# Kernel tuning notes

Hardware: AMD Instinct MI355X
Metric: run time of the kernel (lower is better)

The kernel has to match this reference:

```python
import jax, jax.numpy as jnp
import numpy as np

B, L, D = 1, 1024, 1024
NL = 4            # n_layers
N = 16            # d_state
DI = 2 * D        # d_inner (expand=2)
DTR = (D + 15) // 16  # dt_rank = ceil(d_model/16) = 64
K = 4             # depthwise conv kernel size
EPS = 1e-5


def setup_inputs() -> dict:
    key = jax.random.key(0)
    ks = jax.random.split(key, 8)
    s = lambda k, shp, sc: jax.random.normal(k, shp, jnp.float32) * sc
    x = s(ks[0], (B, L, D), 1.0)
    norm_w = jnp.ones((NL, D), jnp.float32)
    in_w = s(ks[1], (NL, 2 * DI, D), D ** -0.5)          # in_proj (no bias)
    conv_w = s(ks[2], (NL, DI, K), 0.5)                   # depthwise conv1d weight
    conv_b = s(ks[3], (NL, DI), 0.02)                     # conv1d bias
    xproj_w = s(ks[4], (NL, DTR + 2 * N, DI), DI ** -0.5) # x_proj (no bias)
    dt_w = s(ks[5], (NL, DI, DTR), DTR ** -0.5)           # dt_proj weight
    dt_b = jnp.full((NL, DI), 0.1, jnp.float32)           # dt_proj bias (positive-ish delta)
    A_log = jnp.log(jnp.tile(jnp.arange(1, N + 1, dtype=jnp.float32), (NL, DI, 1)))  # [NL, DI, N]
    D_skip = jnp.ones((NL, DI), jnp.float32)
    out_w = s(ks[6], (NL, D, DI), DI ** -0.5)             # out_proj (no bias)
    return dict(x=x, norm_w=norm_w, in_w=in_w, conv_w=conv_w, conv_b=conv_b,
                xproj_w=xproj_w, dt_w=dt_w, dt_b=dt_b, A_log=A_log,
                D_skip=D_skip, out_w=out_w)


def _rmsnorm(x, w):
    return x * jax.lax.rsqrt(jnp.mean(x * x, axis=-1, keepdims=True) + EPS) * w


def _causal_depthwise_conv(u, w, b):
    # u: [B, L, DI], w: [DI, K], b: [DI]; causal (left pad K-1)
    up = jnp.pad(u, ((0, 0), (K - 1, 0), (0, 0)))
    y = b
    for k in range(K):
        y = y + up[:, k:k + L, :] * w[:, k]
    return y


def _selective_scan(dA, dBu, C):
    # dA, dBu: [B, L, DI, N]; C: [B, L, N]
    def step(h, inp):
        a, bu, c = inp
        h = a * h + bu                       # [B, DI, N]
        y = jnp.einsum('bdn,bn->bd', h, c)   # [B, DI]
        return h, y
    h0 = jnp.zeros((dA.shape[0], DI, N), dA.dtype)
    _, ys = jax.lax.scan(step, h0, (dA.transpose(1, 0, 2, 3),
                                    dBu.transpose(1, 0, 2, 3),
                                    C.transpose(1, 0, 2)))
    return ys.transpose(1, 0, 2)             # [B, L, DI]


def _mamba_block(x, p):
    norm_w, in_w, conv_w, conv_b, xproj_w, dt_w, dt_b, A_log, D_skip, out_w = p
    xn = _rmsnorm(x, norm_w)
    xz = jnp.einsum('bld,ed->ble', xn, in_w)             # [B, L, 2*DI]
    u, z = jnp.split(xz, 2, axis=-1)
    u = jax.nn.silu(_causal_depthwise_conv(u, conv_w, conv_b))
    x_dbl = jnp.einsum('bld,ed->ble', u, xproj_w)        # [B, L, DTR+2N]
    dt_r, Bt, Ct = jnp.split(x_dbl, [DTR, DTR + N], axis=-1)
    delta = jax.nn.softplus(jnp.einsum('blr,dr->bld', dt_r, dt_w) + dt_b)  # [B, L, DI]
    A = -jnp.exp(A_log)                                  # [DI, N]
    dA = jnp.exp(delta[..., None] * A)                   # [B, L, DI, N]
    dBu = delta[..., None] * Bt[:, :, None, :] * u[..., None]
    y = _selective_scan(dA, dBu, Ct) + u * D_skip        # [B, L, DI]
    y = y * jax.nn.silu(z)
    return x + jnp.einsum('ble,de->bld', y, out_w)       # residual


def reference(x, norm_w, in_w, conv_w, conv_b, xproj_w, dt_w, dt_b, A_log, D_skip, out_w):
    params = (norm_w, in_w, conv_w, conv_b, xproj_w, dt_w, dt_b, A_log, D_skip, out_w)
    out, _ = jax.lax.scan(lambda h, p: (_mamba_block(h, p), None), x, params)
    return out
```

## Files before the change

kernel.cpp:

```cpp
#include <hip/hip_runtime.h>
#include <hip/hip_bf16.h>
#include <stdint.h>

#define L 1024
#define D 1024
#define NLAYER 4
#define NSTATE 16
#define DI 2048
#define DTR 64
#define KCONV 4
#define XD 96
#define NC 64
#define CT 16
#define KSPLIT 16
#define OSPLIT 4
#define BK 32
#define DIST 4

typedef __attribute__((ext_vector_type(8))) short short8;
typedef __attribute__((ext_vector_type(4))) float floatx4;

__device__ __forceinline__ float siluf(float x) { return x / (1.f + __expf(-x)); }

__device__ __forceinline__ unsigned short f2bf(float x) {
    __hip_bfloat16 b = __float2bfloat16(x);
    return *reinterpret_cast<unsigned short*>(&b);
}

__device__ __forceinline__ short8 pack8(floatx4 a, floatx4 b) {
    short8 o;
    o[0] = (short)f2bf(a.x); o[1] = (short)f2bf(a.y);
    o[2] = (short)f2bf(a.z); o[3] = (short)f2bf(a.w);
    o[4] = (short)f2bf(b.x); o[5] = (short)f2bf(b.y);
    o[6] = (short)f2bf(b.z); o[7] = (short)f2bf(b.w);
    return o;
}

__device__ __forceinline__ void st_dev_u32(uint32_t* p, uint32_t v) {
    __hip_atomic_store(p, v, __ATOMIC_RELAXED, __HIP_MEMORY_SCOPE_AGENT);
}
__device__ __forceinline__ uint32_t ld_dev_u32(const uint32_t* p) {
    return __hip_atomic_load(p, __ATOMIC_RELAXED, __HIP_MEMORY_SCOPE_AGENT);
}
__device__ __forceinline__ void st_dev_u64(void* p, uint64_t v) {
    __hip_atomic_store((unsigned long long*)p, (unsigned long long)v, __ATOMIC_RELAXED, __HIP_MEMORY_SCOPE_AGENT);
}
__device__ __forceinline__ uint64_t ld_dev_u64(const void* p) {
    return (uint64_t)__hip_atomic_load((const unsigned long long*)p, __ATOMIC_RELAXED, __HIP_MEMORY_SCOPE_AGENT);
}
__device__ __forceinline__ float ld_dev_f(const float* p) {
    uint32_t u = ld_dev_u32((const uint32_t*)p);
    union { uint32_t u; float f; } c; c.u = u;
    return c.f;
}
__device__ __forceinline__ void st_dev_f(float* p, float v) {
    union { float f; uint32_t u; } c; c.f = v;
    st_dev_u32((uint32_t*)p, c.u);
}

#define BARRIER_NODRAIN() asm volatile("s_waitcnt lgkmcnt(0)\n\ts_barrier" ::: "memory")

__global__ __launch_bounds__(256) void rmsnorm_kernel(const float* __restrict__ x,
                                                      const float* __restrict__ w,
                                                      __hip_bfloat16* __restrict__ xn,
                                                      uint32_t* __restrict__ flags) {
    if (blockIdx.x == 0) {
#pragma unroll
        for (int i = 0; i < 3; ++i) st_dev_u32(&flags[threadIdx.x + i * 256], 0u);
    }
    int row = blockIdx.x;
    const float* xr = x + (size_t)row * D;
    float v[4];
    float s = 0.f;
#pragma unroll
    for (int i = 0; i < 4; ++i) {
        v[i] = xr[threadIdx.x + i * 256];
        s += v[i] * v[i];
    }
#pragma unroll
    for (int off = 32; off > 0; off >>= 1) s += __shfl_xor(s, off, 64);
    __shared__ float red[4];
    int wave = threadIdx.x >> 6;
    if ((threadIdx.x & 63) == 0) red[wave] = s;
    __syncthreads();
    float inv = rsqrtf((red[0] + red[1] + red[2] + red[3]) * (1.f / D) + 1e-5f);
#pragma unroll
    for (int i = 0; i < 4; ++i) {
        int c = threadIdx.x + i * 256;
        xn[(size_t)row * D + c] = __float2bfloat16(v[i] * inv * w[c]);
    }
}

template <int EPI, int ITERS, bool AF32, int QD>
__global__ __launch_bounds__(256, 2) void gemm_pipe(
    const void* __restrict__ Aptr, int lda,
    const float* __restrict__ Bw, int ldb, int Brows,
    float* __restrict__ C, int ldc, int Nvalid,
    const float* __restrict__ bias) {
    __shared__ __align__(16) __hip_bfloat16 As[2][128 * BK];
    __shared__ __align__(16) __hip_bfloat16 Bs[2][64 * BK];
    int tid = threadIdx.x;
    int wave = tid >> 6, lane = tid & 63;

    int gxy = gridDim.x * gridDim.y;
    int total = gxy * gridDim.z;
    int flat = (blockIdx.z * gridDim.y + blockIdx.y) * gridDim.x + blockIdx.x;
    int bm, bn, bz;
    if ((total & 7) == 0) {
        int lid = (flat & 7) * (total >> 3) + (flat >> 3);
        bz = lid / gxy;
        int rem = lid - bz * gxy;
        bn = rem / gridDim.y;
        bm = rem - bn * gridDim.y;
    } else {
        bm = blockIdx.y; bn = blockIdx.x; bz = blockIdx.z;
    }

    int m0 = bm * 128, n0 = bn * 64;
    int k_base = bz * (ITERS * BK);
    int wr = wave >> 1, wc = wave & 1;
    int srow = lane >> 2, scol = (lane & 3) * 8;
    int q = lane >> 4, r = lane & 15;

    floatx4 acc[4][2] = {};

    int arow0 = m0 + wave * 32 + srow;
    const __hip_bfloat16* gA0 = nullptr; const __hip_bfloat16* gA1 = nullptr;
    const float* gAf0 = nullptr; const float* gAf1 = nullptr;
    if (AF32) {
        gAf0 = (const float*)Aptr + (long)arow0 * lda + scol + k_base;
        gAf1 = gAf0 + (long)16 * lda;
    } else {
        gA0 = (const __hip_bfloat16*)Aptr + (long)arow0 * lda + scol + k_base;
        gA1 = gA0 + (long)16 * lda;
    }
    int bnrow = n0 + wave * 16 + srow;
    const float* gB = Bw + (long)bnrow * ldb + scol + k_base;
    bool bok = bnrow < Brows;

    short8 qa0[QD], qa1[QD];
    floatx4 qaf[AF32 ? QD : 1][4];
    floatx4 qb0[QD] = {}, qb1[QD] = {};

    auto ld = [&](int j) {
        int k0 = j * BK;
        int s = j & (QD - 1);
        if (AF32) {
            qaf[s][0] = *(const floatx4*)(gAf0 + k0);
            qaf[s][1] = *(const floatx4*)(gAf0 + k0 + 4);
            qaf[s][2] = *(const floatx4*)(gAf1 + k0);
            qaf[s][3] = *(const floatx4*)(gAf1 + k0 + 4);
        } else {
            qa0[s] = *(const short8*)(gA0 + k0);
            qa1[s] = *(const short8*)(gA1 + k0);
        }
        if (bok) {
            qb0[s] = *(const floatx4*)(gB + k0);
            qb1[s] = *(const floatx4*)(gB + k0 + 4);
        }
    };
    auto wrstage = [&](int j) {
        int p = j & 1, s = j & (QD - 1);
        if (AF32) {
            *(short8*)(&As[p][(wave * 32 + srow) * BK + scol]) = pack8(qaf[s][0], qaf[s][1]);
            *(short8*)(&As[p][(wave * 32 + 16 + srow) * BK + scol]) = pack8(qaf[s][2], qaf[s][3]);
        } else {
            *(short8*)(&As[p][(wave * 32 + srow) * BK + scol]) = qa0[s];
            *(short8*)(&As[p][(wave * 32 + 16 + srow) * BK + scol]) = qa1[s];
        }
        *(short8*)(&Bs[p][(wave * 16 + srow) * BK + scol]) = pack8(qb0[s], qb1[s]);
    };

#pragma unroll
    for (int j = 0; j < QD; ++j)
        if (j < ITERS) ld(j);
    wrstage(0);

#pragma unroll
    for (int k = 0; k < ITERS; ++k) {
        BARRIER_NODRAIN();
        if (k + QD < ITERS) ld(k + QD);
        if (k + 1 < ITERS) wrstage(k + 1);
        const short* Ap = (const short*)As[k & 1];
        const short* Bp = (const short*)Bs[k & 1];
        short8 af[4], bfr[2];
#pragma unroll
        for (int i = 0; i < 4; ++i)
            af[i] = *(const short8*)(Ap + (wr * 64 + i * 16 + r) * BK + q * 8);
#pragma unroll
        for (int j = 0; j < 2; ++j)
            bfr[j] = *(const short8*)(Bp + (wc * 32 + j * 16 + r) * BK + q * 8);
#pragma unroll
        for (int i = 0; i < 4; ++i)
#pragma unroll
            for (int j = 0; j < 2; ++j)
                acc[i][j] = __builtin_amdgcn_mfma_f32_16x16x32_bf16(af[i], bfr[j], acc[i][j], 0, 0, 0);
    }

#pragma unroll
    for (int i = 0; i < 4; ++i) {
        int mrow = m0 + wr * 64 + i * 16 + q * 4;
#pragma unroll
        for (int j = 0; j < 2; ++j) {
            int ncol = n0 + wc * 32 + j * 16 + r;
            if (ncol < Nvalid) {
#pragma unroll
                for (int rr = 0; rr < 4; ++rr) {
                    float v = acc[i][j][rr];
                    int m = mrow + rr;
                    if (EPI == 1) {
                        v += bias[ncol];
                        v = v > 20.f ? v : log1pf(__expf(v));
                    }
                    if (EPI == 2) atomicAdd(&C[(long)m * ldc + ncol], v);
                    else C[(long)m * ldc + ncol] = v;
                }
            }
        }
    }
}

template <int ITERS>
__global__ __launch_bounds__(256, 1) void gemm128(
    const __hip_bfloat16* __restrict__ A, int lda,
    const float* __restrict__ Bw, int ldb, int Brows,
    float* __restrict__ C, int ldc, long zstride) {
    __shared__ __align__(16) __hip_bfloat16 As[2][128 * BK];
    __shared__ __align__(16) __hip_bfloat16 Bs[2][128 * BK];
    int tid = threadIdx.x;
    int wave = tid >> 6, lane = tid & 63;

    int gxy = gridDim.x * gridDim.y;
    int total = gxy * gridDim.z;
    int flat = (blockIdx.z * gridDim.y + blockIdx.y) * gridDim.x + blockIdx.x;
    int bm, bn, bz;
    if ((total & 7) == 0) {
        int lid = (flat & 7) * (total >> 3) + (flat >> 3);
        bz = lid / gxy;
        int rem = lid - bz * gxy;
        bn = rem / gridDim.y;
        bm = rem - bn * gridDim.y;
    } else {
        bm = blockIdx.y; bn = blockIdx.x; bz = blockIdx.z;
    }

    int m0 = bm * 128, n0 = bn * 128;
    int k_base = bz * (ITERS * BK);
    C += (long)bz * zstride;
    int wr = wave >> 1, wc = wave & 1;
    int srow = lane >> 2, scol = (lane & 3) * 8;
    int q = lane >> 4, r = lane & 15;

    floatx4 acc[4][4] = {};

    const __hip_bfloat16* gA0 = A + (long)(m0 + wave * 32 + srow) * lda + scol + k_base;
    const __hip_bfloat16* gA1 = gA0 + (long)16 * lda;
    int bn0 = n0 + wave * 32 + srow;
    const float* gB0 = Bw + (long)bn0 * ldb + scol + k_base;
    const float* gB1 = gB0 + (long)16 * ldb;
    bool bok0 = bn0 < Brows, bok1 = (bn0 + 16) < Brows;

    short8 qa0[DIST], qa1[DIST];
    floatx4 qb0[DIST] = {}, qb1[DIST] = {}, qb2[DIST] = {}, qb3[DIST] = {};

    auto ld = [&](int j) {
        int k0 = j * BK;
        int s = j & (DIST - 1);
        qa0[s] = *(const short8*)(gA0 + k0);
        qa1[s] = *(const short8*)(gA1 + k0);
        if (bok0) {
            qb0[s] = *(const floatx4*)(gB0 + k0);
            qb1[s] = *(const floatx4*)(gB0 + k0 + 4);
        }
        if (bok1) {
            qb2[s] = *(const floatx4*)(gB1 + k0);
            qb3[s] = *(const floatx4*)(gB1 + k0 + 4);
        }
    };
    auto wrstage = [&](int j) {
        int p = j & 1, s = j & (DIST - 1);
        *(short8*)(&As[p][(wave * 32 + srow) * BK + scol]) = qa0[s];
        *(short8*)(&As[p][(wave * 32 + 16 + srow) * BK + scol]) = qa1[s];
        *(short8*)(&Bs[p][(wave * 32 + srow) * BK + scol]) = pack8(qb0[s], qb1[s]);
        *(short8*)(&Bs[p][(wave * 32 + 16 + srow) * BK + scol]) = pack8(qb2[s], qb3[s]);
    };

#pragma unroll
    for (int j = 0; j < DIST; ++j)
        if (j < ITERS) ld(j);
    wrstage(0);

#pragma unroll
    for (int k = 0; k < ITERS; ++k) {
        BARRIER_NODRAIN();
        if (k + DIST < ITERS) ld(k + DIST);
        if (k + 1 < ITERS) wrstage(k + 1);
        const short* Ap = (const short*)As[k & 1];
        const short* Bp = (const short*)Bs[k & 1];
        short8 af[4], bfr[4];
#pragma unroll
        for (int i = 0; i < 4; ++i)
            af[i] = *(const short8*)(Ap + (wr * 64 + i * 16 + r) * BK + q * 8);
#pragma unroll
        for (int j = 0; j < 4; ++j)
            bfr[j] = *(const short8*)(Bp + (wc * 64 + j * 16 + r) * BK + q * 8);
#pragma unroll
        for (int i = 0; i < 4; ++i)
#pragma unroll
            for (int j = 0; j < 4; ++j)
                acc[i][j] = __builtin_amdgcn_mfma_f32_16x16x32_bf16(af[i], bfr[j], acc[i][j], 0, 0, 0);
    }

#pragma unroll
    for (int i = 0; i < 4; ++i) {
        int mrow = m0 + wr * 64 + i * 16 + q * 4;
#pragma unroll
        for (int j = 0; j < 4; ++j) {
            int ncol = n0 + wc * 64 + j * 16 + r;
#pragma unroll
            for (int rr = 0; rr < 4; ++rr)
                C[(long)(mrow + rr) * ldc + ncol] = acc[i][j][rr];
        }
    }
}

template <int NPART, bool NORM>
__global__ __launch_bounds__(256) void reduce_kernel(const float* __restrict__ part2,
                                                     const float* __restrict__ xin,
                                                     const float* __restrict__ nw,
                                                     float* __restrict__ out,
                                                     __hip_bfloat16* __restrict__ xn) {
    int row = blockIdx.x;
    const float* xr = xin + (size_t)row * D;
    float v[4];
    float ss = 0.f;
#pragma unroll
    for (int i = 0; i < 4; ++i) {
        int c = threadIdx.x + i * 256;
        float s = xr[c];
#pragma unroll
        for (int p = 0; p < NPART; ++p)
            s += part2[(size_t)p * L * D + (size_t)row * D + c];
        v[i] = s;
        out[(size_t)row * D + c] = s;
        ss += s * s;
    }
    if (NORM) {
#pragma unroll
        for (int off = 32; off > 0; off >>= 1) ss += __shfl_xor(ss, off, 64);
        __shared__ float red[4];
        int wave = threadIdx.x >> 6;
        if ((threadIdx.x & 63) == 0) red[wave] = ss;
        __syncthreads();
        float inv = rsqrtf((red[0] + red[1] + red[2] + red[3]) * (1.f / D) + 1e-5f);
#pragma unroll
        for (int i = 0; i < 4; ++i) {
            int c = threadIdx.x + i * 256;
            xn[(size_t)row * D + c] = __float2bfloat16(v[i] * inv * nw[c]);
        }
    }
}

__global__ __launch_bounds__(256) void conv_silu_kernel(const float* __restrict__ xz,
                                                        const float* __restrict__ cw,
                                                        const float* __restrict__ cb,
                                                        __hip_bfloat16* __restrict__ u,
                                                        float* __restrict__ xdbl96) {
    int idx = blockIdx.x * 256 + threadIdx.x;
    if (blockIdx.x < (L * XD) / 256) xdbl96[idx] = 0.f;
    int d = idx & (DI - 1);
    int t = idx >> 11;
    float acc = cb[d];
#pragma unroll
    for (int k = 0; k < KCONV; ++k) {
        int tk = t - (KCONV - 1) + k;
        if (tk >= 0) acc += xz[(size_t)tk * (2 * DI) + d] * cw[d * KCONV + k];
    }
    u[idx] = __float2bfloat16(siluf(acc));
}

__global__ __launch_bounds__(256, 2) void scan_fused(
    const float* __restrict__ delta, const __hip_bfloat16* __restrict__ u,
    const float* __restrict__ xdbl96, const float* __restrict__ Alog,
    const float* __restrict__ xz, const float* __restrict__ Dskip,
    float* __restrict__ Ach, float* __restrict__ Bch,
    __hip_bfloat16* __restrict__ yg,
    uint32_t* __restrict__ flagsA, uint32_t* __restrict__ flagsB, int layer) {
    const int bid = blockIdx.x, tid = threadIdx.x;
    const int g = bid & 7, c = bid >> 3;
    const int d = g * 256 + tid;
    const uint32_t tgt = (uint32_t)(layer + 1);
    __shared__ __align__(16) float Bsh[CT * NSTATE];
    __shared__ __align__(16) float Csh[CT * NSTATE];

    float aval[NSTATE];
    {
        const floatx4* Al4 = (const floatx4*)(Alog + (size_t)d * NSTATE);
#pragma unroll
        for (int n4 = 0; n4 < 4; ++n4) {
            floatx4 t = Al4[n4];
            aval[n4 * 4 + 0] = -__expf(t[0]);
            aval[n4 * 4 + 1] = -__expf(t[1]);
            aval[n4 * 4 + 2] = -__expf(t[2]);
            aval[n4 * 4 + 3] = -__expf(t[3]);
        }
    }

    {
        Bsh[tid] = xdbl96[(size_t)(c * CT + (tid >> 4)) * XD + DTR + (tid & 15)];
        __syncthreads();
        float h[NSTATE], ap[NSTATE];
#pragma unroll
        for (int n = 0; n < NSTATE; ++n) { h[n] = 0.f; ap[n] = 1.f; }
        for (int tt = 0; tt < CT; ++tt) {
            int t = c * CT + tt;
            float dl = delta[(size_t)t * DI + d];
            float uu = __bfloat162float(u[(size_t)t * DI + d]);
            float du = dl * uu;
            const floatx4* Bv = (const floatx4*)(Bsh + tt * NSTATE);
#pragma unroll
            for (int n4 = 0; n4 < 4; ++n4) {
                floatx4 b = Bv[n4];
#pragma unroll
                for (int k = 0; k < 4; ++k) {
                    int n = n4 * 4 + k;
                    float a = __expf(dl * aval[n]);
                    h[n] = a * h[n] + du * b[k];
                    ap[n] *= a;
                }
            }
        }
        float* Ao = Ach + ((size_t)c * DI + d) * NSTATE;
        float* Bo = Bch + ((size_t)c * DI + d) * NSTATE;
#pragma unroll
        for (int n2 = 0; n2 < 8; ++n2) {
            union { float f[2]; uint64_t u; } ca, cb2;
            ca.f[0] = ap[n2 * 2]; ca.f[1] = ap[n2 * 2 + 1];
            cb2.f[0] = h[n2 * 2]; cb2.f[1] = h[n2 * 2 + 1];
            st_dev_u64(Ao + n2 * 2, ca.u);
            st_dev_u64(Bo + n2 * 2, cb2.u);
        }
        asm volatile("s_waitcnt vmcnt(0)" ::: "memory");
        __syncthreads();
        if (tid == 0) st_dev_u32(&flagsA[c * 8 + g], tgt);
    }

    if (bid < 128) {
        int gb = bid >> 4;
        if (tid < 64) {
            while (ld_dev_u32(&flagsA[tid * 8 + gb]) < tgt)
                __builtin_amdgcn_s_sleep(8);
        }
        __syncthreads();
        long i = (long)bid * 256 + tid;
        const long S = (long)DI * NSTATE;
        constexpr int P = 8;
        float ab[P], bb[P];
#pragma unroll
        for (int j = 0; j < P; ++j) {
            ab[j] = ld_dev_f(Ach + (long)j * S + i);
            bb[j] = ld_dev_f(Bch + (long)j * S + i);
        }
        float h = 0.f;
#pragma unroll
        for (int cc = 0; cc < NC; ++cc) {
            float a = ab[cc & (P - 1)];
            float b = bb[cc & (P - 1)];
            st_dev_f(Ach + (long)cc * S + i, h);
            if (cc + P < NC) {
                ab[cc & (P - 1)] = ld_dev_f(Ach + (long)(cc + P) * S + i);
                bb[cc & (P - 1)] = ld_dev_f(Bch + (long)(cc + P) * S + i);
            }
            h = a * h + b;
        }
        asm volatile("s_waitcnt vmcnt(0)" ::: "memory");
        __syncthreads();
        if (tid == 0) st_dev_u32(&flagsB[bid], tgt);
    }

    {
        if (tid < 16) {
            while (ld_dev_u32(&flagsB[g * 16 + tid]) < tgt)
                __builtin_amdgcn_s_sleep(8);
        }
        __syncthreads();
        Bsh[tid] = xdbl96[(size_t)(c * CT + (tid >> 4)) * XD + DTR + (tid & 15)];
        Csh[tid] = xdbl96[(size_t)(c * CT + (tid >> 4)) * XD + DTR + 16 + (tid & 15)];
        __syncthreads();

        float h[NSTATE];
        {
            const float* Hi = Ach + ((size_t)c * DI + d) * NSTATE;
#pragma unroll
            for (int n2 = 0; n2 < 8; ++n2) {
                union { uint64_t u; float f[2]; } cv;
                cv.u = ld_dev_u64(Hi + n2 * 2);
                h[n2 * 2] = cv.f[0]; h[n2 * 2 + 1] = cv.f[1];
            }
        }
        float dsk = Dskip[d];
        for (int tt = 0; tt < CT; ++tt) {
            int t = c * CT + tt;
            float dl = delta[(size_t)t * DI + d];
            float uu = __bfloat162float(u[(size_t)t * DI + d]);
            float du = dl * uu;
            const floatx4* Bv = (const floatx4*)(Bsh + tt * NSTATE);
            const floatx4* Cv = (const floatx4*)(Csh + tt * NSTATE);
            float y = 0.f;
#pragma unroll
            for (int n4 = 0; n4 < 4; ++n4) {
                floatx4 b = Bv[n4];
                floatx4 cc = Cv[n4];
#pragma unroll
                for (int k = 0; k < 4; ++k) {
                    int n = n4 * 4 + k;
                    float a = __expf(dl * aval[n]);
                    h[n] = a * h[n] + du * b[k];
                    y += h[n] * cc[k];
                }
            }
            float z = xz[(size_t)t * (2 * DI) + DI + d];
            yg[(size_t)t * DI + d] = __float2bfloat16((y + uu * dsk) * siluf(z));
        }
    }
}

extern "C" void kernel_launch(void* const* d_in, const int* in_sizes, int n_in,
                              void* d_out, int out_size, void* d_ws, size_t ws_size,
                              hipStream_t stream) {
    const float* x      = (const float*)d_in[0];
    const float* norm_w = (const float*)d_in[1];
    const float* in_w   = (const float*)d_in[2];
    const float* conv_w = (const float*)d_in[3];
    const float* conv_b = (const float*)d_in[4];
    const float* xproj_w= (const float*)d_in[5];
    const float* dt_w   = (const float*)d_in[6];
    const float* dt_b   = (const float*)d_in[7];
    const float* A_log  = (const float*)d_in[8];
    const float* D_skip = (const float*)d_in[9];
    const float* out_w  = (const float*)d_in[10];
    float* out = (float*)d_out;

    uint8_t* wp = (uint8_t*)d_ws;
    auto alloc = [&](size_t bytes) {
        uint8_t* p = wp;
        wp += (bytes + 255) & ~(size_t)255;
        return p;
    };
    __hip_bfloat16* xn_bf   = (__hip_bfloat16*)alloc((size_t)L * D * 2);
    float*          xz      = (float*)alloc((size_t)L * 2 * DI * 4);
    __hip_bfloat16* u_bf    = (__hip_bfloat16*)alloc((size_t)L * DI * 2);
    float*          xdbl96  = (float*)alloc((size_t)L * XD * 4);
    float*          delta   = (float*)alloc((size_t)L * DI * 4);
    __hip_bfloat16* yg_bf   = (__hip_bfloat16*)alloc((size_t)L * DI * 2);
    float*          part2   = (float*)alloc((size_t)OSPLIT * L * D * 4);
    float*          Ach     = (float*)alloc((size_t)NC * DI * NSTATE * 4);
    float*          Bch     = (float*)alloc((size_t)NC * DI * NSTATE * 4);
    uint32_t*       flags   = (uint32_t*)alloc(768 * 4);

    rmsnorm_kernel<<<L, 256, 0, stream>>>(x, norm_w, xn_bf, flags);

    for (int l = 0; l < NLAYER; ++l) {
        const float* xin = (l == 0) ? x : out;

        gemm128<32><<<dim3(4096 / 128, L / 128, 1), 256, 0, stream>>>(
            xn_bf, D, in_w + (size_t)l * 4096 * 1024, D, 4096, xz, 4096, 0);

        conv_silu_kernel<<<L * DI / 256, 256, 0, stream>>>(
            xz, conv_w + (size_t)l * DI * KCONV, conv_b + (size_t)l * DI, u_bf, xdbl96);

        gemm_pipe<2, 2048 / (KSPLIT * BK), false, 4><<<dim3(2, L / 128, KSPLIT), 256, 0, stream>>>(
            u_bf, DI, xproj_w + (size_t)l * 96 * 2048, DI, 96,
            xdbl96, XD, XD, nullptr);

        gemm_pipe<1, 2, true, 2><<<dim3(2048 / 64, L / 128, 1), 256, 0, stream>>>(
            xdbl96, XD, dt_w + (size_t)l * 2048 * 64, DTR, 2048,
            delta, DI, DI, dt_b + (size_t)l * DI);

        scan_fused<<<512, 256, 0, stream>>>(
            delta, u_bf, xdbl96, A_log + (size_t)l * DI * NSTATE, xz,
            D_skip + (size_t)l * DI, Ach, Bch, yg_bf, flags, flags + 512, l);

        gemm128<2048 / (OSPLIT * BK)><<<dim3(1024 / 128, L / 128, OSPLIT), 256, 0, stream>>>(
            yg_bf, DI, out_w + (size_t)l * 1024 * 2048, DI, 1024,
            part2, D, (long)L * D);

        if (l < NLAYER - 1)
            reduce_kernel<OSPLIT, true><<<L, 256, 0, stream>>>(
                part2, xin, norm_w + (size_t)(l + 1) * D, out, xn_bf);
        else
            reduce_kernel<OSPLIT, false><<<L, 256, 0, stream>>>(
                part2, xin, nullptr, out, nullptr);
    }
}
```

Baseline: 742.3 us.

## Replace atomic split-K x_proj with partial buffers summed by consumers

```diff
diff --git a/kernel.cpp b/kernel.cpp
--- a/kernel.cpp
+++ b/kernel.cpp
@@ -12,7 +12,7 @@
 #define XD 96
 #define NC 64
 #define CT 16
-#define KSPLIT 16
+#define KSPLIT 8
 #define OSPLIT 4
 #define BK 32
 #define DIST 4
@@ -91,11 +91,11 @@
     }
 }
 
-template <int EPI, int ITERS, bool AF32, int QD>
+template <int EPI, bool ASUM, int ITERS, int QD>
 __global__ __launch_bounds__(256, 2) void gemm_pipe(
-    const void* __restrict__ Aptr, int lda,
+    const void* __restrict__ Aptr, int lda, long astride,
     const float* __restrict__ Bw, int ldb, int Brows,
-    float* __restrict__ C, int ldc, int Nvalid,
+    float* __restrict__ C, int ldc, int Nvalid, long zstride,
     const float* __restrict__ bias) {
     __shared__ __align__(16) __hip_bfloat16 As[2][128 * BK];
     __shared__ __align__(16) __hip_bfloat16 Bs[2][64 * BK];
@@ -118,6 +118,7 @@
 
     int m0 = bm * 128, n0 = bn * 64;
     int k_base = bz * (ITERS * BK);
+    C += (long)bz * zstride;
     int wr = wave >> 1, wc = wave & 1;
     int srow = lane >> 2, scol = (lane & 3) * 8;
     int q = lane >> 4, r = lane & 15;
@@ -127,7 +128,7 @@
     int arow0 = m0 + wave * 32 + srow;
     const __hip_bfloat16* gA0 = nullptr; const __hip_bfloat16* gA1 = nullptr;
     const float* gAf0 = nullptr; const float* gAf1 = nullptr;
-    if (AF32) {
+    if (ASUM) {
         gAf0 = (const float*)Aptr + (long)arow0 * lda + scol + k_base;
         gAf1 = gAf0 + (long)16 * lda;
     } else {
@@ -139,17 +140,25 @@
     bool bok = bnrow < Brows;
 
     short8 qa0[QD], qa1[QD];
-    floatx4 qaf[AF32 ? QD : 1][4];
+    floatx4 qaf[ASUM ? QD : 1][4];
     floatx4 qb0[QD] = {}, qb1[QD] = {};
 
     auto ld = [&](int j) {
         int k0 = j * BK;
         int s = j & (QD - 1);
-        if (AF32) {
-            qaf[s][0] = *(const floatx4*)(gAf0 + k0);
-            qaf[s][1] = *(const floatx4*)(gAf0 + k0 + 4);
-            qaf[s][2] = *(const floatx4*)(gAf1 + k0);
-            qaf[s][3] = *(const floatx4*)(gAf1 + k0 + 4);
+        if (ASUM) {
+            floatx4 t0 = *(const floatx4*)(gAf0 + k0);
+            floatx4 t1 = *(const floatx4*)(gAf0 + k0 + 4);
+            floatx4 t2 = *(const floatx4*)(gAf1 + k0);
+            floatx4 t3 = *(const floatx4*)(gAf1 + k0 + 4);
+#pragma unroll
+            for (int sp = 1; sp < KSPLIT; ++sp) {
+                t0 += *(const floatx4*)(gAf0 + sp * astride + k0);
+                t1 += *(const floatx4*)(gAf0 + sp * astride + k0 + 4);
+                t2 += *(const floatx4*)(gAf1 + sp * astride + k0);
+                t3 += *(const floatx4*)(gAf1 + sp * astride + k0 + 4);
+            }
+            qaf[s][0] = t0; qaf[s][1] = t1; qaf[s][2] = t2; qaf[s][3] = t3;
         } else {
             qa0[s] = *(const short8*)(gA0 + k0);
             qa1[s] = *(const short8*)(gA1 + k0);
@@ -161,7 +170,7 @@
     };
     auto wrstage = [&](int j) {
         int p = j & 1, s = j & (QD - 1);
-        if (AF32) {
+        if (ASUM) {
             *(short8*)(&As[p][(wave * 32 + srow) * BK + scol]) = pack8(qaf[s][0], qaf[s][1]);
             *(short8*)(&As[p][(wave * 32 + 16 + srow) * BK + scol]) = pack8(qaf[s][2], qaf[s][3]);
         } else {
@@ -212,8 +221,7 @@
                         v += bias[ncol];
                         v = v > 20.f ? v : log1pf(__expf(v));
                     }
-                    if (EPI == 2) atomicAdd(&C[(long)m * ldc + ncol], v);
-                    else C[(long)m * ldc + ncol] = v;
+                    C[(long)m * ldc + ncol] = v;
                 }
             }
         }
@@ -364,10 +372,8 @@
 __global__ __launch_bounds__(256) void conv_silu_kernel(const float* __restrict__ xz,
                                                         const float* __restrict__ cw,
                                                         const float* __restrict__ cb,
-                                                        __hip_bfloat16* __restrict__ u,
-                                                        float* __restrict__ xdbl96) {
+                                                        __hip_bfloat16* __restrict__ u) {
     int idx = blockIdx.x * 256 + threadIdx.x;
-    if (blockIdx.x < (L * XD) / 256) xdbl96[idx] = 0.f;
     int d = idx & (DI - 1);
     int t = idx >> 11;
     float acc = cb[d];
@@ -381,8 +387,9 @@
 
 __global__ __launch_bounds__(256, 2) void scan_fused(
     const float* __restrict__ delta, const __hip_bfloat16* __restrict__ u,
-    const float* __restrict__ xdbl96, const float* __restrict__ Alog,
-    const float* __restrict__ xz, const float* __restrict__ Dskip,
+    const float* __restrict__ part,
+    const float* __restrict__ Alog, const float* __restrict__ xz,
+    const float* __restrict__ Dskip,
     float* __restrict__ Ach, float* __restrict__ Bch,
     __hip_bfloat16* __restrict__ yg,
     uint32_t* __restrict__ flagsA, uint32_t* __restrict__ flagsB, int layer) {
@@ -392,6 +399,18 @@
     const uint32_t tgt = (uint32_t)(layer + 1);
     __shared__ __align__(16) float Bsh[CT * NSTATE];
     __shared__ __align__(16) float Csh[CT * NSTATE];
+    __shared__ __align__(16) float bounce[4096];
+
+    for (int s2 = tid; s2 < CT * 32; s2 += 256) {
+        int tt = s2 >> 5, col = s2 & 31;
+        float sum = 0.f;
+#pragma unroll
+        for (int sp = 0; sp < KSPLIT; ++sp)
+            sum += part[(size_t)sp * L * XD + (size_t)(c * CT + tt) * XD + DTR + col];
+        if (col < 16) Bsh[tt * NSTATE + col] = sum;
+        else          Csh[tt * NSTATE + (col - 16)] = sum;
+    }
+    __syncthreads();
 
     float aval[NSTATE];
     {
@@ -407,8 +426,6 @@
     }
 
     {
-        Bsh[tid] = xdbl96[(size_t)(c * CT + (tid >> 4)) * XD + DTR + (tid & 15)];
-        __syncthreads();
         float h[NSTATE], ap[NSTATE];
 #pragma unroll
         for (int n = 0; n < NSTATE; ++n) { h[n] = 0.f; ap[n] = 1.f; }
@@ -430,15 +447,34 @@
                 }
             }
         }
-        float* Ao = Ach + ((size_t)c * DI + d) * NSTATE;
-        float* Bo = Bch + ((size_t)c * DI + d) * NSTATE;
-#pragma unroll
-        for (int n2 = 0; n2 < 8; ++n2) {
-            union { float f[2]; uint64_t u; } ca, cb2;
-            ca.f[0] = ap[n2 * 2]; ca.f[1] = ap[n2 * 2 + 1];
-            cb2.f[0] = h[n2 * 2]; cb2.f[1] = h[n2 * 2 + 1];
-            st_dev_u64(Ao + n2 * 2, ca.u);
-            st_dev_u64(Bo + n2 * 2, cb2.u);
+        uint64_t* gA = (uint64_t*)(Ach + ((size_t)c * DI + g * 256) * NSTATE);
+        uint64_t* gB = (uint64_t*)(Bch + ((size_t)c * DI + g * 256) * NSTATE);
+        {
+            floatx4* bl = (floatx4*)(bounce + tid * NSTATE);
+#pragma unroll
+            for (int n4 = 0; n4 < 4; ++n4)
+                bl[n4] = floatx4{ap[n4 * 4], ap[n4 * 4 + 1], ap[n4 * 4 + 2], ap[n4 * 4 + 3]};
+        }
+        __syncthreads();
+        {
+            const uint64_t* bb = (const uint64_t*)bounce;
+#pragma unroll
+            for (int w = 0; w < 8; ++w)
+                st_dev_u64(gA + w * 256 + tid, bb[w * 256 + tid]);
+        }
+        __syncthreads();
+        {
+            floatx4* bl = (floatx4*)(bounce + tid * NSTATE);
+#pragma unroll
+            for (int n4 = 0; n4 < 4; ++n4)
+                bl[n4] = floatx4{h[n4 * 4], h[n4 * 4 + 1], h[n4 * 4 + 2], h[n4 * 4 + 3]};
+        }
+        __syncthreads();
+        {
+            const uint64_t* bb = (const uint64_t*)bounce;
+#pragma unroll
+            for (int w = 0; w < 8; ++w)
+                st_dev_u64(gB + w * 256 + tid, bb[w * 256 + tid]);
         }
         asm volatile("s_waitcnt vmcnt(0)" ::: "memory");
         __syncthreads();
@@ -484,19 +520,21 @@
                 __builtin_amdgcn_s_sleep(8);
         }
         __syncthreads();
-        Bsh[tid] = xdbl96[(size_t)(c * CT + (tid >> 4)) * XD + DTR + (tid & 15)];
-        Csh[tid] = xdbl96[(size_t)(c * CT + (tid >> 4)) * XD + DTR + 16 + (tid & 15)];
-        __syncthreads();
-
+        {
+            const uint64_t* gH = (const uint64_t*)(Ach + ((size_t)c * DI + g * 256) * NSTATE);
+            uint64_t hb[8];
+#pragma unroll
+            for (int w = 0; w < 8; ++w) hb[w] = ld_dev_u64(gH + w * 256 + tid);
+            uint64_t* bb = (uint64_t*)bounce;
+#pragma unroll
+            for (int w = 0; w < 8; ++w) bb[w * 256 + tid] = hb[w];
+        }
+        __syncthreads();
         float h[NSTATE];
         {
-            const float* Hi = Ach + ((size_t)c * DI + d) * NSTATE;
-#pragma unroll
-            for (int n2 = 0; n2 < 8; ++n2) {
-                union { uint64_t u; float f[2]; } cv;
-                cv.u = ld_dev_u64(Hi + n2 * 2);
-                h[n2 * 2] = cv.f[0]; h[n2 * 2 + 1] = cv.f[1];
-            }
+            const float* bl = bounce + tid * NSTATE;
+#pragma unroll
+            for (int n = 0; n < NSTATE; ++n) h[n] = bl[n];
         }
         float dsk = Dskip[d];
         for (int tt = 0; tt < CT; ++tt) {
@@ -550,7 +588,7 @@
     __hip_bfloat16* xn_bf   = (__hip_bfloat16*)alloc((size_t)L * D * 2);
     float*          xz      = (float*)alloc((size_t)L * 2 * DI * 4);
     __hip_bfloat16* u_bf    = (__hip_bfloat16*)alloc((size_t)L * DI * 2);
-    float*          xdbl96  = (float*)alloc((size_t)L * XD * 4);
+    float*          part    = (float*)alloc((size_t)KSPLIT * L * XD * 4);
     float*          delta   = (float*)alloc((size_t)L * DI * 4);
     __hip_bfloat16* yg_bf   = (__hip_bfloat16*)alloc((size_t)L * DI * 2);
     float*          part2   = (float*)alloc((size_t)OSPLIT * L * D * 4);
@@ -567,18 +605,18 @@
             xn_bf, D, in_w + (size_t)l * 4096 * 1024, D, 4096, xz, 4096, 0);
 
         conv_silu_kernel<<<L * DI / 256, 256, 0, stream>>>(
-            xz, conv_w + (size_t)l * DI * KCONV, conv_b + (size_t)l * DI, u_bf, xdbl96);
-
-        gemm_pipe<2, 2048 / (KSPLIT * BK), false, 4><<<dim3(2, L / 128, KSPLIT), 256, 0, stream>>>(
-            u_bf, DI, xproj_w + (size_t)l * 96 * 2048, DI, 96,
-            xdbl96, XD, XD, nullptr);
-
-        gemm_pipe<1, 2, true, 2><<<dim3(2048 / 64, L / 128, 1), 256, 0, stream>>>(
-            xdbl96, XD, dt_w + (size_t)l * 2048 * 64, DTR, 2048,
-            delta, DI, DI, dt_b + (size_t)l * DI);
+            xz, conv_w + (size_t)l * DI * KCONV, conv_b + (size_t)l * DI, u_bf);
+
+        gemm_pipe<0, false, 8, 4><<<dim3(2, L / 128, KSPLIT), 256, 0, stream>>>(
+            u_bf, DI, 0, xproj_w + (size_t)l * 96 * 2048, DI, 96,
+            part, XD, XD, (long)L * XD, nullptr);
+
+        gemm_pipe<1, true, 2, 2><<<dim3(2048 / 64, L / 128, 1), 256, 0, stream>>>(
+            part, XD, (long)L * XD, dt_w + (size_t)l * 2048 * 64, DTR, 2048,
+            delta, DI, DI, 0, dt_b + (size_t)l * DI);
 
         scan_fused<<<512, 256, 0, stream>>>(
-            delta, u_bf, xdbl96, A_log + (size_t)l * DI * NSTATE, xz,
+            delta, u_bf, part, A_log + (size_t)l * DI * NSTATE, xz,
             D_skip + (size_t)l * DI, Ach, Bch, yg_bf, flags, flags + 512, l);
 
         gemm128<2048 / (OSPLIT * BK)><<<dim3(1024 / 128, L / 128, OSPLIT), 256, 0, stream>>>(
```

Measured after the change: 675.7 us. 9.0% less time.
